# Kernel tuning notes

Hardware: AMD Instinct MI355X
Metric: run time of the kernel (lower is better)

## Reference

```python
import jax, jax.numpy as jnp
import numpy as np
import math

E, H, KH, F = 2048, 32, 8, 8192
HD = E // H          # 64
KV = KH * HD         # 512
B, S = 2, 2048
EPS = 1e-5


def _rope_table(seq_len, head_dim, base=10000.0):
    inv = 1.0 / (base ** (np.arange(0, head_dim, 2, dtype=np.float32) / head_dim))
    t = np.arange(seq_len, dtype=np.float32)
    fr = np.outer(t, inv)                               # [S, HD/2]
    return jnp.asarray(np.stack([np.cos(fr), np.sin(fr)], axis=-1))  # [S, HD/2, 2]


def setup_inputs() -> dict:
    key = jax.random.key(0)
    ks = jax.random.split(key, 8)
    x = jax.random.normal(ks[0], (B, S, E), dtype=jnp.float32)
    attention_mask = jnp.tril(jnp.ones((1, 1, S, S), dtype=bool))  # causal
    freqs_cis = _rope_table(S, HD)                                  # [S, 32, 2]
    sc = 0.02
    w_qkv = jax.random.normal(ks[1], (E + 2 * KV, E), dtype=jnp.float32) * sc
    w_o = jax.random.normal(ks[2], (E, E), dtype=jnp.float32) * sc
    w1 = jax.random.normal(ks[3], (F, E), dtype=jnp.float32) * sc
    w3 = jax.random.normal(ks[4], (F, E), dtype=jnp.float32) * sc
    w2 = jax.random.normal(ks[5], (E, F), dtype=jnp.float32) * sc
    attn_norm_w = jnp.ones((E,), dtype=jnp.float32)
    ff_norm_w = jnp.ones((E,), dtype=jnp.float32)
    return {"x": x, "attention_mask": attention_mask, "freqs_cis": freqs_cis,
            "w_qkv": w_qkv, "w_o": w_o, "w1": w1, "w2": w2, "w3": w3,
            "attn_norm_w": attn_norm_w, "ff_norm_w": ff_norm_w}


def _rmsnorm(x, w):
    xf = x.astype(jnp.float32)
    n = xf * jax.lax.rsqrt(jnp.mean(xf * xf, axis=-1, keepdims=True) + EPS)
    return n.astype(x.dtype) * w


def _apply_rope(x, freqs_cis):
    # x: [B, h, S, HD]; freqs_cis: [S, HD/2, 2] broadcasting over B, h
    xf = x.astype(jnp.float32).reshape(*x.shape[:-1], -1, 2)
    c, s = freqs_cis[..., 0], freqs_cis[..., 1]
    x0, x1 = xf[..., 0], xf[..., 1]
    out = jnp.stack([x0 * c - x1 * s, x1 * c + x0 * s], axis=-1)
    return out.reshape(x.shape).astype(x.dtype)


def reference(x, attention_mask, freqs_cis, w_qkv, w_o, w1, w2, w3, attn_norm_w, ff_norm_w):
    bs, seq = x.shape[:2]
    h = _rmsnorm(x, attn_norm_w)
    qkv = h @ w_qkv.T                                   # [B, S, E + 2*KV]
    q, k, v = jnp.split(qkv, [E, E + KV], axis=-1)
    q = q.reshape(bs, seq, H, HD).transpose(0, 2, 1, 3)   # [B, H, S, HD]
    k = k.reshape(bs, seq, KH, HD).transpose(0, 2, 1, 3)  # [B, KH, S, HD]
    v = v.reshape(bs, seq, KH, HD).transpose(0, 2, 1, 3)
    q = _apply_rope(q, freqs_cis)
    k = _apply_rope(k, freqs_cis)
    rep = H // KH
    k = jnp.repeat(k, rep, axis=1)                        # [B, H, S, HD]
    v = jnp.repeat(v, rep, axis=1)
    score = jnp.einsum('bhqd,bhkd->bhqk', q, k) / math.sqrt(HD)
    score = jnp.where(attention_mask, score, -jnp.inf)
    attn = jax.nn.softmax(score, axis=-1)
    o = jnp.einsum('bhqk,bhkd->bhqd', attn, v)
    o = o.transpose(0, 2, 1, 3).reshape(bs, seq, E) @ w_o.T
    h2 = x + o
    g = _rmsnorm(h2, ff_norm_w)
    ff = (jax.nn.silu(g @ w1.T) * (g @ w3.T)) @ w2.T
    return h2 + ff
```

## Files before the change

kernel.cpp:

```cpp
#include <hip/hip_runtime.h>
#include <hip/hip_bf16.h>
#include <cstdint>
#include <cstddef>

typedef __bf16 bf16;
typedef __bf16 bf16x2 __attribute__((ext_vector_type(2)));
typedef __bf16 bf16x4 __attribute__((ext_vector_type(4)));
typedef __bf16 bf16x8 __attribute__((ext_vector_type(8)));
typedef float f32x4 __attribute__((ext_vector_type(4)));
typedef float f32x16 __attribute__((ext_vector_type(16)));

#define EDIM 2048
#define SEQ  2048
#define BATCH 2
#define NH   32
#define NKV  8
#define HD   64
#define FF   8192
#define NTOK 4096
#define QKVN 3072

__device__ __forceinline__ void gld_lds16(const void* gp, void* lp) {
    __builtin_amdgcn_global_load_lds(
        (__attribute__((address_space(1))) void*)(gp),
        (__attribute__((address_space(3))) void*)(lp), 16, 0, 0);
}

__global__ __launch_bounds__(256)
void cvt_f32_bf16(const float* __restrict__ in, bf16* __restrict__ out, long n4) {
    long i = (long)blockIdx.x * blockDim.x + threadIdx.x;
    long stride = (long)gridDim.x * blockDim.x;
    for (; i < n4; i += stride) {
        float4 v = ((const float4*)in)[i];
        bf16x4 o;
        o[0] = (bf16)v.x; o[1] = (bf16)v.y; o[2] = (bf16)v.z; o[3] = (bf16)v.w;
        ((bf16x4*)out)[i] = o;
    }
}

__global__ __launch_bounds__(256)
void rmsnorm_bf16(const float* __restrict__ x, const float* __restrict__ w,
                  bf16* __restrict__ out) {
    __shared__ float red[4];
    const int row = blockIdx.x;
    const long base = (long)row * EDIM;
    const int t = threadIdx.x;
    float4 v0 = *(const float4*)(x + base + t * 4);
    float4 v1 = *(const float4*)(x + base + 1024 + t * 4);
    float ss = v0.x*v0.x + v0.y*v0.y + v0.z*v0.z + v0.w*v0.w
             + v1.x*v1.x + v1.y*v1.y + v1.z*v1.z + v1.w*v1.w;
    #pragma unroll
    for (int off = 1; off < 64; off <<= 1) ss += __shfl_xor(ss, off, 64);
    if ((t & 63) == 0) red[t >> 6] = ss;
    __syncthreads();
    float tot = red[0] + red[1] + red[2] + red[3];
    float inv = rsqrtf(tot * (1.0f / EDIM) + 1e-5f);
    float4 w0 = *(const float4*)(w + t * 4);
    float4 w1 = *(const float4*)(w + 1024 + t * 4);
    bf16x4 o0, o1;
    o0[0] = (bf16)(v0.x * inv * w0.x); o0[1] = (bf16)(v0.y * inv * w0.y);
    o0[2] = (bf16)(v0.z * inv * w0.z); o0[3] = (bf16)(v0.w * inv * w0.w);
    o1[0] = (bf16)(v1.x * inv * w1.x); o1[1] = (bf16)(v1.y * inv * w1.y);
    o1[2] = (bf16)(v1.z * inv * w1.z); o1[3] = (bf16)(v1.w * inv * w1.w);
    *(bf16x4*)(out + base + t * 4) = o0;
    *(bf16x4*)(out + base + 1024 + t * 4) = o1;
}

template<int EPI>
__global__ __launch_bounds__(256, 2)
void gemm_nt(const bf16* __restrict__ A, const bf16* __restrict__ B,
             void* __restrict__ Cv, const float* __restrict__ res,
             int M, int N, int K) {
    __shared__ bf16 As[128 * 32];
    __shared__ bf16 Bs[128 * 32];
    const int tid = threadIdx.x;
    const int lane = tid & 63;
    const int wave = tid >> 6;
    const int wm = (wave >> 1) * 64;
    const int wn = (wave & 1) * 64;
    const int bm = blockIdx.y * 128;
    const int bn = blockIdx.x * 128;
    const int lrow = lane & 15;
    const int koff = (lane >> 4) * 8;

    f32x4 acc[4][4] = {};

    for (int k0 = 0; k0 < K; k0 += 32) {
        __syncthreads();
        #pragma unroll
        for (int t = 0; t < 2; ++t) {
            int c = tid + t * 256;
            int r = c >> 2;
            int kc = (c & 3) * 8;
            gld_lds16(A + (long)(bm + r) * K + k0 + kc, As + c * 8);
            gld_lds16(B + (long)(bn + r) * K + k0 + kc, Bs + c * 8);
        }
        __syncthreads();
        bf16x8 af[4], bfr[4];
        #pragma unroll
        for (int t = 0; t < 4; ++t) {
            af[t]  = *(const bf16x8*)(As + (wm + t * 16 + lrow) * 32 + koff);
            bfr[t] = *(const bf16x8*)(Bs + (wn + t * 16 + lrow) * 32 + koff);
        }
        #pragma unroll
        for (int i = 0; i < 4; ++i)
            #pragma unroll
            for (int j = 0; j < 4; ++j)
                acc[i][j] = __builtin_amdgcn_mfma_f32_16x16x32_bf16(af[i], bfr[j], acc[i][j], 0, 0, 0);
    }

    const int row0 = bm + wm + (lane >> 4) * 4;
    const int col0 = bn + wn + (lane & 15);
    #pragma unroll
    for (int i = 0; i < 4; ++i) {
        #pragma unroll
        for (int j = 0; j < 4; ++j) {
            int col = col0 + j * 16;
            #pragma unroll
            for (int r = 0; r < 4; ++r) {
                long idx = (long)(row0 + i * 16 + r) * N + col;
                float v = acc[i][j][r];
                if (EPI == 0) {
                    ((float*)Cv)[idx] = v;
                } else if (EPI == 1) {
                    ((bf16*)Cv)[idx] = (bf16)v;
                } else if (EPI == 2) {
                    ((float*)Cv)[idx] = v + res[idx];
                } else {
                    float u = (float)((bf16*)Cv)[idx];
                    float sl = u / (1.0f + __expf(-u));
                    ((bf16*)Cv)[idx] = (bf16)(sl * v);
                }
            }
        }
    }
}

__global__ __launch_bounds__(256)
void rope_prep(const bf16* __restrict__ qkv, const float* __restrict__ fr,
               bf16* __restrict__ Qo, bf16* __restrict__ Ko) {
    const int row = blockIdx.x;
    const int b = row >> 11, s = row & 2047;
    const int t = threadIdx.x;
    const long rbase = (long)row * QKVN;
    #pragma unroll
    for (int i = 0; i < 4; ++i) {
        int p = t + i * 256;
        int hh = p >> 5, d = p & 31;
        bf16x2 xv = *(const bf16x2*)(qkv + rbase + hh * 64 + 2 * d);
        float x0 = (float)xv[0], x1 = (float)xv[1];
        float2 cs = *(const float2*)(fr + (long)(s * 32 + d) * 2);
        bf16x2 o;
        o[0] = (bf16)((x0 * cs.x - x1 * cs.y) * 0.125f);
        o[1] = (bf16)((x1 * cs.x + x0 * cs.y) * 0.125f);
        *(bf16x2*)(Qo + ((long)(b * NH + hh) * SEQ + s) * HD + 2 * d) = o;
    }
    {
        int kh = t >> 5, d = t & 31;
        bf16x2 xv = *(const bf16x2*)(qkv + rbase + EDIM + kh * 64 + 2 * d);
        float x0 = (float)xv[0], x1 = (float)xv[1];
        float2 cs = *(const float2*)(fr + (long)(s * 32 + d) * 2);
        bf16x2 o;
        o[0] = (bf16)(x0 * cs.x - x1 * cs.y);
        o[1] = (bf16)(x1 * cs.x + x0 * cs.y);
        *(bf16x2*)(Ko + ((long)(b * NKV + kh) * SEQ + s) * HD + 2 * d) = o;
    }
}

__global__ __launch_bounds__(256)
void v_prep(const bf16* __restrict__ qkv, bf16* __restrict__ Vt) {
    __shared__ bf16 tile[64 * 72];
    const int blk = blockIdx.x;
    const int b = blk >> 8;
    const int kvh = (blk >> 5) & 7;
    const int st = blk & 31;
    const int t = threadIdx.x;
    #pragma unroll
    for (int i = 0; i < 2; ++i) {
        int c = t + i * 256;
        int kk = c >> 3, hdo = (c & 7) * 8;
        bf16x8 v = *(const bf16x8*)(qkv + (long)(b * SEQ + st * 64 + kk) * QKVN + 2560 + kvh * 64 + hdo);
        *(bf16x8*)(tile + kk * 72 + hdo) = v;
    }
    __syncthreads();
    const long obase = ((long)(b * NKV + kvh) * 32 + st) * 4096;
    #pragma unroll
    for (int i = 0; i < 2; ++i) {
        int c = t + i * 256;
        int hd = c >> 3, ko = (c & 7) * 8;
        bf16x8 v;
        #pragma unroll
        for (int j = 0; j < 8; ++j) v[j] = tile[(ko + j) * 72 + hd];
        *(bf16x8*)(Vt + obase + hd * 64 + ko) = v;
    }
}

__global__ __launch_bounds__(256, 4)
void attn_fwd(const bf16* __restrict__ Q, const bf16* __restrict__ K,
              const bf16* __restrict__ Vt, bf16* __restrict__ Out) {
    __shared__ bf16 Ps[4][32][40];
    const int tid = threadIdx.x, lane = tid & 63, w = tid >> 6;
    const int qt = blockIdx.x;
    const int bh = blockIdx.y;
    const int b = bh >> 5, h = bh & 31;
    const int kvh = h >> 2;
    const int ql = lane & 31;
    const int hh = lane >> 5;
    const int q3 = ql & 3;
    const int q0 = qt * 128 + w * 32;
    const long qbase  = ((long)(b * NH + h) * SEQ + q0) * HD;
    const long kvbase = ((long)(b * NKV + kvh) * SEQ) * HD;
    bf16* Pw = &Ps[w][0][0];

    bf16x8 qa[4];
    #pragma unroll
    for (int ds = 0; ds < 4; ++ds)
        qa[ds] = *(const bf16x8*)(Q + qbase + (long)ql * HD + ds * 16 + hh * 8);

    f32x16 oacc[2] = {};
    float mi = -1e30f, li = 0.f;

    const int ntiles = qt * 4 + w + 1;
    for (int kt = 0; kt < ntiles; ++kt) {
        const bf16* Kt = K + kvbase + (long)kt * (32 * HD);
        f32x16 s = {};
        #pragma unroll
        for (int ds = 0; ds < 4; ++ds) {
            bf16x8 ka = *(const bf16x8*)(Kt + ql * HD + ds * 16 + hh * 8);
            s = __builtin_amdgcn_mfma_f32_32x32x16_bf16(ka, qa[ds], s, 0, 0, 0);
        }
        if (kt == ntiles - 1) {
            #pragma unroll
            for (int r = 0; r < 16; ++r) {
                int kk = kt * 32 + (r & 3) + 8 * (r >> 2) + 4 * hh;
                if (kk > q0 + ql) s[r] = -1e30f;
            }
        }
        float tmax = s[0];
        #pragma unroll
        for (int r = 1; r < 16; ++r) tmax = fmaxf(tmax, s[r]);
        tmax = fmaxf(tmax, __shfl_xor(tmax, 32, 64));
        if (!__all(tmax <= mi)) {
            float mnew = fmaxf(mi, tmax);
            float alpha = __expf(mi - mnew);
            li *= alpha;
            #pragma unroll
            for (int r = 0; r < 16; ++r) { oacc[0][r] *= alpha; oacc[1][r] *= alpha; }
            mi = mnew;
        }
        float psum = 0.f;
        #pragma unroll
        for (int g2 = 0; g2 < 4; ++g2) {
            bf16x4 pw;
            #pragma unroll
            for (int j = 0; j < 4; ++j) {
                float p = __expf(s[g2 * 4 + j] - mi);
                psum += p;
                pw[j] = (bf16)p;
            }
            *(bf16x4*)(Pw + ql * 40 + ((g2 ^ q3) << 3) + 4 * hh) = pw;
        }
        psum += __shfl_xor(psum, 32, 64);
        li += psum;
        bf16x8 p0 = *(const bf16x8*)(Pw + ql * 40 + ((hh ^ q3) << 3));
        bf16x8 p1 = *(const bf16x8*)(Pw + ql * 40 + (((2 + hh) ^ q3) << 3));
        const bf16* Vtt = Vt + kvbase + (long)(kt >> 1) * 4096 + (kt & 1) * 32;
        #pragma unroll
        for (int t = 0; t < 2; ++t) {
            bf16x8 va0 = *(const bf16x8*)(Vtt + (t * 32 + ql) * 64 + hh * 8);
            bf16x8 va1 = *(const bf16x8*)(Vtt + (t * 32 + ql) * 64 + 16 + hh * 8);
            oacc[t] = __builtin_amdgcn_mfma_f32_32x32x16_bf16(va0, p0, oacc[t], 0, 0, 0);
            oacc[t] = __builtin_amdgcn_mfma_f32_32x32x16_bf16(va1, p1, oacc[t], 0, 0, 0);
        }
    }

    float inv = 1.0f / li;
    const long obase = ((long)b * SEQ + q0 + ql) * EDIM + h * 64;
    #pragma unroll
    for (int t = 0; t < 2; ++t)
        #pragma unroll
        for (int rg = 0; rg < 4; ++rg) {
            bf16x4 o4;
            #pragma unroll
            for (int j = 0; j < 4; ++j) o4[j] = (bf16)(oacc[t][rg * 4 + j] * inv);
            *(bf16x4*)(Out + obase + t * 32 + rg * 8 + hh * 4) = o4;
        }
}

extern "C" void kernel_launch(void* const* d_in, const int* in_sizes, int n_in,
                              void* d_out, int out_size, void* d_ws, size_t ws_size,
                              hipStream_t stream) {
    const float* x    = (const float*)d_in[0];
    const float* fr   = (const float*)d_in[2];
    const float* wqkv = (const float*)d_in[3];
    const float* wo   = (const float*)d_in[4];
    const float* w1   = (const float*)d_in[5];
    const float* w2   = (const float*)d_in[6];
    const float* w3   = (const float*)d_in[7];
    const float* anw  = (const float*)d_in[8];
    const float* fnw  = (const float*)d_in[9];
    float* out = (float*)d_out;

    const size_t SZ_WQKV = (size_t)QKVN * EDIM;
    const size_t SZ_WO   = (size_t)EDIM * EDIM;
    const size_t SZ_WFF  = (size_t)FF * EDIM;
    const size_t B_WQKV  = SZ_WQKV * 2;
    const size_t B_WO    = SZ_WO * 2;
    const size_t B_WFF   = SZ_WFF * 2;
    const size_t B_HATTN = (size_t)NTOK * EDIM * 2;
    const size_t B_QKV   = (size_t)NTOK * QKVN * 2;
    const size_t B_SCR   = (size_t)NTOK * EDIM * 4;
    const size_t B_FF1   = (size_t)NTOK * FF * 2;
    const size_t NEED = B_WQKV + B_WO + 3 * B_WFF + B_HATTN + B_QKV + B_SCR + B_FF1;
    if (ws_size < NEED) return;

    char* ws = (char*)d_ws;
    size_t off = 0;
    auto alloc = [&](size_t bytes) -> void* {
        void* p = ws + off;
        off += (bytes + 255) & ~(size_t)255;
        return p;
    };
    bf16* wqkv_b = (bf16*)alloc(B_WQKV);
    bf16* wo_b   = (bf16*)alloc(B_WO);
    bf16* w1_b   = (bf16*)alloc(B_WFF);
    bf16* w3_b   = (bf16*)alloc(B_WFF);
    bf16* w2_b   = (bf16*)alloc(B_WFF);
    bf16* h_attn = (bf16*)alloc(B_HATTN);
    bf16* qkv_g  = (bf16*)alloc(B_QKV);
    char* scr    = (char*)alloc(B_SCR);
    bf16* Qb  = (bf16*)scr;
    bf16* Kb  = (bf16*)(scr + (size_t)BATCH * NH * SEQ * HD * 2);
    bf16* Vtb = (bf16*)(scr + (size_t)BATCH * (NH + NKV) * SEQ * HD * 2);
    float* h2 = (float*)scr;
    bf16* ff1 = (bf16*)alloc(B_FF1);
    bf16* g_b = qkv_g;

    cvt_f32_bf16<<<512, 256, 0, stream>>>(wqkv, wqkv_b, (long)(SZ_WQKV / 4));
    cvt_f32_bf16<<<512, 256, 0, stream>>>(wo,   wo_b,   (long)(SZ_WO / 4));
    cvt_f32_bf16<<<512, 256, 0, stream>>>(w1,   w1_b,   (long)(SZ_WFF / 4));
    cvt_f32_bf16<<<512, 256, 0, stream>>>(w3,   w3_b,   (long)(SZ_WFF / 4));
    cvt_f32_bf16<<<512, 256, 0, stream>>>(w2,   w2_b,   (long)(SZ_WFF / 4));
    rmsnorm_bf16<<<NTOK, 256, 0, stream>>>(x, anw, h_attn);
    gemm_nt<1><<<dim3(QKVN / 128, NTOK / 128), 256, 0, stream>>>(
        h_attn, wqkv_b, qkv_g, nullptr, NTOK, QKVN, EDIM);
    rope_prep<<<NTOK, 256, 0, stream>>>(qkv_g, fr, Qb, Kb);
    v_prep<<<BATCH * NKV * (SEQ / 64), 256, 0, stream>>>(qkv_g, Vtb);
    attn_fwd<<<dim3(SEQ / 128, BATCH * NH), 256, 0, stream>>>(Qb, Kb, Vtb, h_attn);
    gemm_nt<2><<<dim3(EDIM / 128, NTOK / 128), 256, 0, stream>>>(
        h_attn, wo_b, h2, x, NTOK, EDIM, EDIM);
    rmsnorm_bf16<<<NTOK, 256, 0, stream>>>(h2, fnw, g_b);
    gemm_nt<1><<<dim3(FF / 128, NTOK / 128), 256, 0, stream>>>(
        g_b, w1_b, ff1, nullptr, NTOK, FF, EDIM);
    gemm_nt<3><<<dim3(FF / 128, NTOK / 128), 256, 0, stream>>>(
        g_b, w3_b, ff1, nullptr, NTOK, FF, EDIM);
    gemm_nt<2><<<dim3(EDIM / 128, NTOK / 128), 256, 0, stream>>>(
        ff1, w2_b, out, h2, NTOK, EDIM, FF);
    (void)in_sizes; (void)n_in; (void)out_size; (void)ws_size;
}
```

Before: 1.202 ms.

## Process 64-key tiles with batched K/V prefetch in attention kernel

The attention loop now walks 64-key tiles. It loads all K and V fragments for both 32-key halves up front, then runs two softmax/MFMA sub-steps, and skips the second half when it lies fully past the causal limit. This is meant to hide global load latency behind compute. The grid is transposed so heads vary fastest, which groups blocks sharing a query tile and changes L2 reuse of K/V. The P-tile LDS swizzle is changed to reduce bank conflicts. Launch bounds drop from 4 to 3 waves to make room for the extra registers, which lowers occupancy.

```diff
diff --git a/kernel.cpp b/kernel.cpp
--- a/kernel.cpp
+++ b/kernel.cpp
@@ -195,19 +195,20 @@
     }
 }
 
-__global__ __launch_bounds__(256, 4)
+__global__ __launch_bounds__(256, 3)
 void attn_fwd(const bf16* __restrict__ Q, const bf16* __restrict__ K,
               const bf16* __restrict__ Vt, bf16* __restrict__ Out) {
     __shared__ bf16 Ps[4][32][40];
     const int tid = threadIdx.x, lane = tid & 63, w = tid >> 6;
-    const int qt = blockIdx.x;
-    const int bh = blockIdx.y;
+    const int bh = blockIdx.x;
+    const int qt = blockIdx.y;
     const int b = bh >> 5, h = bh & 31;
     const int kvh = h >> 2;
     const int ql = lane & 31;
     const int hh = lane >> 5;
-    const int q3 = ql & 3;
+    const int sw = (ql ^ (ql >> 3)) & 3;
     const int q0 = qt * 128 + w * 32;
+    const int qmax = q0 + 31;
     const long qbase  = ((long)(b * NH + h) * SEQ + q0) * HD;
     const long kvbase = ((long)(b * NKV + kvh) * SEQ) * HD;
     bf16* Pw = &Ps[w][0][0];
@@ -220,57 +221,71 @@
     f32x16 oacc[2] = {};
     float mi = -1e30f, li = 0.f;
 
-    const int ntiles = qt * 4 + w + 1;
-    for (int kt = 0; kt < ntiles; ++kt) {
-        const bf16* Kt = K + kvbase + (long)kt * (32 * HD);
-        f32x16 s = {};
-        #pragma unroll
-        for (int ds = 0; ds < 4; ++ds) {
-            bf16x8 ka = *(const bf16x8*)(Kt + ql * HD + ds * 16 + hh * 8);
-            s = __builtin_amdgcn_mfma_f32_32x32x16_bf16(ka, qa[ds], s, 0, 0, 0);
-        }
-        if (kt == ntiles - 1) {
-            #pragma unroll
-            for (int r = 0; r < 16; ++r) {
-                int kk = kt * 32 + (r & 3) + 8 * (r >> 2) + 4 * hh;
-                if (kk > q0 + ql) s[r] = -1e30f;
-            }
-        }
-        float tmax = s[0];
-        #pragma unroll
-        for (int r = 1; r < 16; ++r) tmax = fmaxf(tmax, s[r]);
-        tmax = fmaxf(tmax, __shfl_xor(tmax, 32, 64));
-        if (!__all(tmax <= mi)) {
-            float mnew = fmaxf(mi, tmax);
-            float alpha = __expf(mi - mnew);
-            li *= alpha;
-            #pragma unroll
-            for (int r = 0; r < 16; ++r) { oacc[0][r] *= alpha; oacc[1][r] *= alpha; }
-            mi = mnew;
-        }
-        float psum = 0.f;
-        #pragma unroll
-        for (int g2 = 0; g2 < 4; ++g2) {
-            bf16x4 pw;
-            #pragma unroll
-            for (int j = 0; j < 4; ++j) {
-                float p = __expf(s[g2 * 4 + j] - mi);
-                psum += p;
-                pw[j] = (bf16)p;
-            }
-            *(bf16x4*)(Pw + ql * 40 + ((g2 ^ q3) << 3) + 4 * hh) = pw;
-        }
-        psum += __shfl_xor(psum, 32, 64);
-        li += psum;
-        bf16x8 p0 = *(const bf16x8*)(Pw + ql * 40 + ((hh ^ q3) << 3));
-        bf16x8 p1 = *(const bf16x8*)(Pw + ql * 40 + (((2 + hh) ^ q3) << 3));
-        const bf16* Vtt = Vt + kvbase + (long)(kt >> 1) * 4096 + (kt & 1) * 32;
-        #pragma unroll
-        for (int t = 0; t < 2; ++t) {
-            bf16x8 va0 = *(const bf16x8*)(Vtt + (t * 32 + ql) * 64 + hh * 8);
-            bf16x8 va1 = *(const bf16x8*)(Vtt + (t * 32 + ql) * 64 + 16 + hh * 8);
-            oacc[t] = __builtin_amdgcn_mfma_f32_32x32x16_bf16(va0, p0, oacc[t], 0, 0, 0);
-            oacc[t] = __builtin_amdgcn_mfma_f32_32x32x16_bf16(va1, p1, oacc[t], 0, 0, 0);
+    const int nt64 = qt * 2 + 1 + (w >> 1);
+    for (int kt = 0; kt < nt64; ++kt) {
+        const bf16* Kt  = K  + kvbase + (long)kt * (64 * HD);
+        const bf16* Vtt = Vt + kvbase + (long)kt * 4096;
+        bf16x8 ka[2][4], va[2][2][2];
+        #pragma unroll
+        for (int h2 = 0; h2 < 2; ++h2)
+            #pragma unroll
+            for (int ds = 0; ds < 4; ++ds)
+                ka[h2][ds] = *(const bf16x8*)(Kt + (h2 * 32 + ql) * HD + ds * 16 + hh * 8);
+        #pragma unroll
+        for (int h2 = 0; h2 < 2; ++h2)
+            #pragma unroll
+            for (int t = 0; t < 2; ++t)
+                #pragma unroll
+                for (int c = 0; c < 2; ++c)
+                    va[h2][t][c] = *(const bf16x8*)(Vtt + (t * 32 + ql) * 64 + h2 * 32 + c * 16 + hh * 8);
+        const bool lastt = (kt == nt64 - 1);
+        #pragma unroll
+        for (int h2 = 0; h2 < 2; ++h2) {
+            if (h2 == 1 && kt * 64 + 32 > qmax) break;
+            f32x16 s = {};
+            #pragma unroll
+            for (int ds = 0; ds < 4; ++ds)
+                s = __builtin_amdgcn_mfma_f32_32x32x16_bf16(ka[h2][ds], qa[ds], s, 0, 0, 0);
+            if (lastt) {
+                #pragma unroll
+                for (int r = 0; r < 16; ++r) {
+                    int kk = kt * 64 + h2 * 32 + (r & 3) + 8 * (r >> 2) + 4 * hh;
+                    if (kk > q0 + ql) s[r] = -1e30f;
+                }
+            }
+            float tmax = s[0];
+            #pragma unroll
+            for (int r = 1; r < 16; ++r) tmax = fmaxf(tmax, s[r]);
+            tmax = fmaxf(tmax, __shfl_xor(tmax, 32, 64));
+            if (!__all(tmax <= mi)) {
+                float mnew = fmaxf(mi, tmax);
+                float alpha = __expf(mi - mnew);
+                li *= alpha;
+                #pragma unroll
+                for (int r = 0; r < 16; ++r) { oacc[0][r] *= alpha; oacc[1][r] *= alpha; }
+                mi = mnew;
+            }
+            float psum = 0.f;
+            #pragma unroll
+            for (int g2 = 0; g2 < 4; ++g2) {
+                bf16x4 pw;
+                #pragma unroll
+                for (int j = 0; j < 4; ++j) {
+                    float p = __expf(s[g2 * 4 + j] - mi);
+                    psum += p;
+                    pw[j] = (bf16)p;
+                }
+                *(bf16x4*)(Pw + ql * 40 + ((g2 ^ sw) << 3) + 4 * hh) = pw;
+            }
+            psum += __shfl_xor(psum, 32, 64);
+            li += psum;
+            bf16x8 p0 = *(const bf16x8*)(Pw + ql * 40 + ((hh ^ sw) << 3));
+            bf16x8 p1 = *(const bf16x8*)(Pw + ql * 40 + (((2 + hh) ^ sw) << 3));
+            #pragma unroll
+            for (int t = 0; t < 2; ++t) {
+                oacc[t] = __builtin_amdgcn_mfma_f32_32x32x16_bf16(va[h2][t][0], p0, oacc[t], 0, 0, 0);
+                oacc[t] = __builtin_amdgcn_mfma_f32_32x32x16_bf16(va[h2][t][1], p1, oacc[t], 0, 0, 0);
+            }
         }
     }
 
@@ -346,7 +361,7 @@
         h_attn, wqkv_b, qkv_g, nullptr, NTOK, QKVN, EDIM);
     rope_prep<<<NTOK, 256, 0, stream>>>(qkv_g, fr, Qb, Kb);
     v_prep<<<BATCH * NKV * (SEQ / 64), 256, 0, stream>>>(qkv_g, Vtb);
-    attn_fwd<<<dim3(SEQ / 128, BATCH * NH), 256, 0, stream>>>(Qb, Kb, Vtb, h_attn);
+    attn_fwd<<<dim3(BATCH * NH, SEQ / 128), 256, 0, stream>>>(Qb, Kb, Vtb, h_attn);
     gemm_nt<2><<<dim3(EDIM / 128, NTOK / 128), 256, 0, stream>>>(
         h_attn, wo_b, h2, x, NTOK, EDIM, EDIM);
     rmsnorm_bf16<<<NTOK, 256, 0, stream>>>(h2, fnw, g_b);
```

Measured after the change: 1.119 ms. -7.0%, faster.
